# Performance work log

Measured on AMD Instinct MI355X. Metric: run time of the kernel, lower is better.

## Reference

```python
import jax, jax.numpy as jnp
import numpy as np

BLOCK = 4096  # bitsandbytes blockwise quantization block size
VOCAB, DIM = 50400, 4096  # GPT-J 6B word-token embedding


def setup_inputs() -> dict:
    key = jax.random.key(0)
    k1, k2, k3, k4 = jax.random.split(key, 4)
    weight = jax.random.randint(k1, (VOCAB, DIM), 0, 256, dtype=jnp.int32)  # int8 codes (stored as int32 indices)
    n_blocks = (VOCAB * DIM) // BLOCK
    absmax = jax.random.uniform(k2, (n_blocks,), dtype=jnp.float32)  # per-block scale
    code = jax.random.normal(k3, (256,), dtype=jnp.float32)  # int8 -> float lookup table
    inp = jax.random.randint(k4, (4, 2048), 0, VOCAB, dtype=jnp.int32)  # token ids
    return {"input": inp, "weight": weight, "absmax": absmax, "code": code}


def reference(input, weight, absmax, code):
    # dequantize_blockwise: out[i] = code[q[i]] * absmax[i // BLOCK]
    V, D = weight.shape
    blocks = weight.reshape(-1, BLOCK)           # [n_blocks, BLOCK]
    weight_deq = (code[blocks] * absmax[:, None]).reshape(V, D)  # [V, D] fp32
    # F.embedding gather
    return weight_deq[input]                     # [B, S, D]
```

## Files before the change

### kernel.cpp

```cpp
#include <hip/hip_runtime.h>
#include <hip/hip_bf16.h>


#define DIM 4096

__global__ __launch_bounds__(256) void bnb_embed_kernel(
    const int* __restrict__ tokens,
    const int* __restrict__ weight,
    const float* __restrict__ absmax,
    const float* __restrict__ code,
    float* __restrict__ out,
    int n_tokens)
{
    __shared__ float lut[256];
    lut[threadIdx.x] = code[threadIdx.x];
    __syncthreads();

    const int tokIdx = blockIdx.x;
    if (tokIdx >= n_tokens) return;

    const int t = tokens[tokIdx];
    const float scale = absmax[t];

    const int4* __restrict__ wrow = (const int4*)(weight + (size_t)t * DIM);
    float4* __restrict__ orow = (float4*)(out + (size_t)tokIdx * DIM);

#pragma unroll
    for (int i = 0; i < 4; ++i) {
        const int idx = threadIdx.x + i * 256;
        const int4 q = wrow[idx];
        float4 o;
        o.x = lut[q.x & 255] * scale;
        o.y = lut[q.y & 255] * scale;
        o.z = lut[q.z & 255] * scale;
        o.w = lut[q.w & 255] * scale;
        orow[idx] = o;
    }
}

extern "C" void kernel_launch(void* const* d_in, const int* in_sizes, int n_in,
                              void* d_out, int out_size, void* d_ws, size_t ws_size,
                              hipStream_t stream)
{
    const int*   tokens = (const int*)d_in[0];
    const int*   weight = (const int*)d_in[1];
    const float* absmax = (const float*)d_in[2];
    const float* code   = (const float*)d_in[3];
    float*       out    = (float*)d_out;

    const int n_tokens = in_sizes[0];
    bnb_embed_kernel<<<n_tokens, 256, 0, stream>>>(tokens, weight, absmax, code, out, n_tokens);
}
```

Baseline: 937.8 us.

## Map one wavefront per token with batched loads and nontemporal stores

The kernel now gives each 64-lane wavefront a whole token row instead of giving each 256-thread block one row, using a grid-stride loop with the grid capped at 2048 blocks. Each lane issues all 16 of its int4 row loads before doing any lookups, which puts more memory requests in flight per wave. Output writes use nontemporal stores so the streamed result bypasses cache retention. The token id is made wave-uniform with readfirstlane. In exchange, each lane holds more registers, and with 8192 tokens there are fewer waves in total than before, which could cut occupancy.

```diff
diff --git a/kernel.cpp b/kernel.cpp
--- a/kernel.cpp
+++ b/kernel.cpp
@@ -1,8 +1,9 @@
 #include <hip/hip_runtime.h>
-#include <hip/hip_bf16.h>
 
 
 #define DIM 4096
+
+typedef float  fx4 __attribute__((ext_vector_type(4)));
 
 __global__ __launch_bounds__(256) void bnb_embed_kernel(
     const int* __restrict__ tokens,
@@ -16,25 +17,32 @@
     lut[threadIdx.x] = code[threadIdx.x];
     __syncthreads();
 
-    const int tokIdx = blockIdx.x;
-    if (tokIdx >= n_tokens) return;
+    const int wave = threadIdx.x >> 6;
+    const int lane = threadIdx.x & 63;
+    const int waveGlobal  = blockIdx.x * 4 + wave;
+    const int nWavesTotal = gridDim.x * 4;
 
-    const int t = tokens[tokIdx];
-    const float scale = absmax[t];
+    for (int tok = waveGlobal; tok < n_tokens; tok += nWavesTotal) {
+        const int   t     = __builtin_amdgcn_readfirstlane(tokens[tok]);
+        const float scale = absmax[t];
 
-    const int4* __restrict__ wrow = (const int4*)(weight + (size_t)t * DIM);
-    float4* __restrict__ orow = (float4*)(out + (size_t)tokIdx * DIM);
+        const int4* __restrict__ wrow = (const int4*)(weight + (size_t)t * DIM);
+        fx4* __restrict__ orow        = (fx4*)(out + (size_t)tok * DIM);
+
+        int4 q[16];
+#pragma unroll
+        for (int i = 0; i < 16; ++i)
+            q[i] = wrow[lane + i * 64];
 
 #pragma unroll
-    for (int i = 0; i < 4; ++i) {
-        const int idx = threadIdx.x + i * 256;
-        const int4 q = wrow[idx];
-        float4 o;
-        o.x = lut[q.x & 255] * scale;
-        o.y = lut[q.y & 255] * scale;
-        o.z = lut[q.z & 255] * scale;
-        o.w = lut[q.w & 255] * scale;
-        orow[idx] = o;
+        for (int i = 0; i < 16; ++i) {
+            fx4 o;
+            o.x = lut[q[i].x & 255] * scale;
+            o.y = lut[q[i].y & 255] * scale;
+            o.z = lut[q[i].z & 255] * scale;
+            o.w = lut[q[i].w & 255] * scale;
+            __builtin_nontemporal_store(o, &orow[lane + i * 64]);
+        }
     }
 }
 
@@ -49,5 +57,10 @@
     float*       out    = (float*)d_out;
 
     const int n_tokens = in_sizes[0];
-    bnb_embed_kernel<<<n_tokens, 256, 0, stream>>>(tokens, weight, absmax, code, out, n_tokens);
+
+    int blocks = (n_tokens + 3) / 4;
+    if (blocks > 2048) blocks = 2048;
+    if (blocks < 1)    blocks = 1;
+
+    bnb_embed_kernel<<<blocks, 256, 0, stream>>>(tokens, weight, absmax, code, out, n_tokens);
 }
```

Measured after the change: 941.2 us. No clear change (+0.4%).
